# Kernel optimization log

Measured on AMD Instinct MI355X. Metric: run time of the kernel, lower is better.

## Reference

```python
import jax, jax.numpy as jnp
import numpy as np
import math

EMBED_DIM = 128
NUM_HEADS = 16
HEAD_DIM = EMBED_DIM // NUM_HEADS  # = 8 = n_wires of the quantum circuit


def setup_inputs() -> dict:
    key = jax.random.key(0)
    k1, k2, k3 = jax.random.split(key, 3)
    B, S = 4, 2048
    x = jax.random.normal(k1, (B, S, EMBED_DIM), dtype=jnp.float32)
    # shared trainable RX angles of the single q_layer (applied to every head)
    theta = jax.random.normal(k2, (HEAD_DIM,), dtype=jnp.float32)
    w_out = jax.random.normal(k3, (EMBED_DIM, EMBED_DIM), dtype=jnp.float32) / math.sqrt(EMBED_DIM)
    mask = jnp.ones((B, S), dtype=jnp.int32)
    return {"x": x, "theta": theta, "w_out": w_out, "mask": mask}


def quantum_linear(x_head, theta):
    # Circuit: RX(x_i) encode + RX(theta_i) on wire i, CNOT chain (i, i+1),
    # then <Z_j>. For product state |psi_i> = RX(phi_i)|0>, <Z_i> = cos(phi_i),
    # and the CNOT chain gives final <Z_j> = prod_{i<=j} cos(phi_i).
    phi = x_head + theta  # [..., D] broadcast over leading dims
    return jnp.cumprod(jnp.cos(phi), axis=-1)


def reference(x, theta, w_out, mask):
    B, S, E = x.shape
    H, D = NUM_HEADS, HEAD_DIM
    xs = x.reshape(B, S, H, D)
    q = quantum_linear(xs, theta).transpose(0, 2, 1, 3)  # [B, H, S, D]; k = v = q
    scores = jnp.einsum("bhsd,bhtd->bhst", q, q) / math.sqrt(D)
    scores = jnp.where(mask[:, None, None, :] == 0, -1e9, scores)
    probs = jax.nn.softmax(scores, axis=-1)  # dropout is identity in eval
    attn = jnp.einsum("bhst,bhtd->bhsd", probs, q)
    attn = attn.transpose(0, 2, 1, 3).reshape(B, S, E)
    return attn @ w_out.T
```

## Files before the change

kernel.cpp:

```cpp
#include <hip/hip_runtime.h>
#include <hip/hip_bf16.h>
#include <hip/hip_fp16.h>

#define NB 4
#define NS 2048
#define NE 128
#define NH 16
#define ND 8

#define THALF 1024
#define NCH 32
#define VSTRIDE 1032
#define VGSTR 2056

typedef __attribute__((ext_vector_type(8))) _Float16 half8;
typedef __attribute__((ext_vector_type(4))) _Float16 half4;
typedef __attribute__((ext_vector_type(4))) float f32x4;

__device__ __forceinline__ unsigned int pkrtz(float a, float b) {
    typedef __fp16 fp16v2 __attribute__((ext_vector_type(2)));
    union { fp16v2 h; unsigned int u; } v;
    v.h = __builtin_amdgcn_cvt_pkrtz(a, b);
    return v.u;
}
__device__ __forceinline__ unsigned short f2h(float a) {
    return __half_as_ushort(__float2half(a));
}
__device__ __forceinline__ half8 mk_half8(unsigned u0, unsigned u1,
                                          unsigned u2, unsigned u3) {
    union { half8 h; unsigned u[4]; } v;
    v.u[0] = u0; v.u[1] = u1; v.u[2] = u2; v.u[3] = u3;
    return v.h;
}

__device__ __forceinline__ void qrow(const float* __restrict__ xp,
                                     const float* th, float* p) {
    float4 a = *(const float4*)xp, c = *(const float4*)(xp + 4);
    float t = 1.f;
    t *= cosf(a.x + th[0]); p[0] = t;
    t *= cosf(a.y + th[1]); p[1] = t;
    t *= cosf(a.z + th[2]); p[2] = t;
    t *= cosf(a.w + th[3]); p[3] = t;
    t *= cosf(c.x + th[4]); p[4] = t;
    t *= cosf(c.y + th[5]); p[5] = t;
    t *= cosf(c.z + th[6]); p[6] = t;
    t *= cosf(c.w + th[7]); p[7] = t;
}

__global__ __launch_bounds__(256) void qgen_kernel(
        const float* __restrict__ x,
        const float* __restrict__ theta,
        const int* __restrict__ mask,
        const float* __restrict__ w,
        unsigned short* __restrict__ qg,
        unsigned short* __restrict__ vtg,
        unsigned short* __restrict__ wf16) {
    const int gid = blockIdx.x * 256 + threadIdx.x;
    const int bh = gid >> 10;
    const int b = bh >> 4, h = bh & (NH - 1);
    const int j = gid & 1023;
    const int s0 = 2 * j;
    const float SC = 0.71421629f;

    if (blockIdx.x == 0) {
        for (int i = threadIdx.x; i < 2048; i += 256) {
            const float* wp = w + i * 8;
            float4 a = *(const float4*)wp, c = *(const float4*)(wp + 4);
            uint4 pk;
            pk.x = pkrtz(a.x, a.y); pk.y = pkrtz(a.z, a.w);
            pk.z = pkrtz(c.x, c.y); pk.w = pkrtz(c.z, c.w);
            *(uint4*)&wf16[i * 8] = pk;
        }
    }

    float th[ND];
#pragma unroll
    for (int d = 0; d < ND; d++) th[d] = theta[d];

    float p0[ND], p1[ND];
    qrow(x + ((size_t)(b * NS + s0) * NE + h * ND), th, p0);
    qrow(x + ((size_t)(b * NS + s0 + 1) * NE + h * ND), th, p1);
    const float mz0 = mask[b * NS + s0] ? 1.f : 0.f;
    const float mz1 = mask[b * NS + s0 + 1] ? 1.f : 0.f;

    uint4 qa, qb;
    qa.x = pkrtz(p0[0] * SC, p0[1] * SC);
    qa.y = pkrtz(p0[2] * SC, p0[3] * SC);
    qa.z = pkrtz(p0[4] * SC, p0[5] * SC);
    qa.w = pkrtz(p0[6] * SC, p0[7] * SC);
    qb.x = pkrtz(p1[0] * SC, p1[1] * SC);
    qb.y = pkrtz(p1[2] * SC, p1[3] * SC);
    qb.z = pkrtz(p1[4] * SC, p1[5] * SC);
    qb.w = pkrtz(p1[6] * SC, p1[7] * SC);
    *(uint4*)&qg[((size_t)bh * NS + s0) * ND] = qa;
    *(uint4*)&qg[((size_t)bh * NS + s0 + 1) * ND] = qb;

    const int H = s0 >> 10, r0 = s0 & 1023;
    const int chs = r0 >> 5, u = (r0 & 31) >> 1;
    const int i = (u & 1) | (((u >> 3) & 1) << 1) | (((u >> 1) & 3) << 2);
    const int col = H * THALF + chs * 32 + 2 * i;
    unsigned short* vb = vtg + (size_t)bh * 9 * VGSTR + col;
#pragma unroll
    for (int d = 0; d < ND; d++)
        *(unsigned int*)&vb[d * VGSTR] = pkrtz(p0[d] * mz0, p1[d] * mz1);
    *(unsigned int*)&vb[8 * VGSTR] = pkrtz(mz0, mz1);
}

__global__ __launch_bounds__(512) void attn_kernel(
        const unsigned short* __restrict__ qg,
        const unsigned short* __restrict__ vtg,
        unsigned short* __restrict__ mid) {
    __shared__ unsigned short qhl[THALF * ND + 24];
    __shared__ unsigned short vT[9 * VSTRIDE];

    const int bid = blockIdx.x;
    const int bh = bid >> 4;
    const int b = bh >> 4, h = bh & (NH - 1);
    const int msix = bid & 15;
    const int tid = threadIdx.x;

    const int wave = tid >> 6, lane = tid & 63;
    const int quad = lane >> 4, l15 = lane & 15;
    const int mbase = msix * 128 + wave * 16;

    if (tid < 24) qhl[THALF * ND + tid] = 0;

    half4 hz4 = {0, 0, 0, 0};
    const unsigned short* qmrow = qg + ((size_t)bh * NS + mbase + l15) * ND
                                + (quad < 2 ? quad * 4 : 0);
    half4 bm0 = (quad < 2) ? *(const half4*)qmrow : hz4;

    const int vrow = (l15 < 9) ? l15 : 8;
    const unsigned short* vbase = &vT[vrow * VSTRIDE];

    f32x4 O0 = {0.f, 0.f, 0.f, 0.f};
    const f32x4 zc = {0.f, 0.f, 0.f, 0.f};

    for (int p = 0; p < 2; p++) {
        {
            const uint4* qs = (const uint4*)(qg + ((size_t)bh * NS + p * THALF) * ND);
            uint4* qd = (uint4*)qhl;
            qd[tid] = qs[tid];
            qd[tid + 512] = qs[tid + 512];
        }
        {
            const unsigned short* vs = vtg + (size_t)bh * 9 * VGSTR + p * THALF;
            for (int jj = tid; jj < 1152; jj += 512) {
                int d = jj >> 7, c = (jj & 127) << 3;
                *(uint4*)&vT[d * VSTRIDE + c] = *(const uint4*)&vs[d * VGSTR + c];
            }
        }
        __syncthreads();

        for (int ch = 0; ch < NCH; ch++) {
            int tb = ch * 32;
            half4 at0 = *(const half4*)&qhl[(tb + l15) * ND + quad * 4];
            half4 at1 = *(const half4*)&qhl[(tb + 16 + l15) * ND + quad * 4];
            half8 vf  = *(const half8*)&vbase[tb + quad * 8];

            f32x4 s00 = __builtin_amdgcn_mfma_f32_16x16x16f16(at0, bm0, zc, 0, 0, 0);
            f32x4 s10 = __builtin_amdgcn_mfma_f32_16x16x16f16(at1, bm0, zc, 0, 0, 0);

            half8 pA0 = mk_half8(
                pkrtz(__builtin_amdgcn_exp2f(s00[0]), __builtin_amdgcn_exp2f(s00[1])),
                pkrtz(__builtin_amdgcn_exp2f(s00[2]), __builtin_amdgcn_exp2f(s00[3])),
                pkrtz(__builtin_amdgcn_exp2f(s10[0]), __builtin_amdgcn_exp2f(s10[1])),
                pkrtz(__builtin_amdgcn_exp2f(s10[2]), __builtin_amdgcn_exp2f(s10[3])));

            O0 = __builtin_amdgcn_mfma_f32_16x16x32_f16(pA0, vf, O0, 0, 0, 0);
        }
        __syncthreads();
    }

#pragma unroll
    for (int r = 0; r < 4; r++) {
        float lsum = __shfl(O0[r], (lane & 48) | 8, 64);
        float v = O0[r] / lsum;
        if (l15 < ND) {
            int m = mbase + quad * 4 + r;
            mid[(size_t)(b * NS + m) * NE + h * ND + l15] = f2h(v);
        }
    }
}

__global__ __launch_bounds__(512) void proj_kernel(
        const unsigned short* __restrict__ mid,
        const unsigned short* __restrict__ wf16,
        float* __restrict__ out) {
    const int rb = blockIdx.x * 16;
    const int tid = threadIdx.x;
    const int wavei = tid >> 6, lane = tid & 63;
    const int quad = lane >> 4, l15 = lane & 15;
    const int n0 = wavei * 16;

    f32x4 acc = {0.f, 0.f, 0.f, 0.f};
#pragma unroll
    for (int kt = 0; kt < 4; kt++) {
        half8 af = *(const half8*)&mid[(size_t)(rb + l15) * NE + kt * 32 + quad * 8];
        half8 bf = *(const half8*)&wf16[(n0 + l15) * NE + kt * 32 + quad * 8];
        acc = __builtin_amdgcn_mfma_f32_16x16x32_f16(af, bf, acc, 0, 0, 0);
    }
#pragma unroll
    for (int r = 0; r < 4; r++)
        out[(size_t)(rb + quad * 4 + r) * NE + n0 + l15] = acc[r];
}

extern "C" void kernel_launch(void* const* d_in, const int* in_sizes, int n_in,
                              void* d_out, int out_size, void* d_ws, size_t ws_size,
                              hipStream_t stream) {
    const float* x     = (const float*)d_in[0];
    const float* theta = (const float*)d_in[1];
    const float* w_out = (const float*)d_in[2];
    const int*   mask  = (const int*)d_in[3];
    float* out = (float*)d_out;

    unsigned short* mid16 = (unsigned short*)d_ws;
    unsigned short* qg   = mid16 + (size_t)NB * NS * NE;
    unsigned short* vtg  = qg + (size_t)NB * NH * NS * ND;
    unsigned short* wf16 = vtg + (size_t)NB * NH * 9 * VGSTR;

    qgen_kernel<<<NB * NH * NS / 2 / 256, 256, 0, stream>>>(x, theta, mask, w_out,
                                                            qg, vtg, wf16);
    attn_kernel<<<NB * NH * 16, 512, 0, stream>>>(qg, vtg, mid16);
    proj_kernel<<<NB * NS / 16, 512, 0, stream>>>(mid16, wf16, out);
}
```

Before: 103.9 us.

## Switch attention to 32x32x16 MFMA tiles reading K/V directly from global

The attention kernel now uses 32x32x16 f16 MFMA instructions: each wave handles 32 query rows and processes 32 keys per step over 64 steps. LDS staging and the __syncthreads barriers are dropped, and the 256-thread block loads Q and V fragments straight from global memory, relying on L1/L2 caching. The V-transpose layout written by qgen is reorganized into 16-key blocks of 144 halfs so each lane's fragment is contiguous. Global loads in the inner loop may add latency compared with LDS reads, but the larger tiles do more work per instruction and the block no longer has to synchronize.

```diff
diff --git a/kernel.cpp b/kernel.cpp
--- a/kernel.cpp
+++ b/kernel.cpp
@@ -8,14 +8,12 @@
 #define NH 16
 #define ND 8
 
-#define THALF 1024
-#define NCH 32
-#define VSTRIDE 1032
-#define VGSTR 2056
+#define VT_BLK 144
+#define VT_BH (128 * VT_BLK)
 
 typedef __attribute__((ext_vector_type(8))) _Float16 half8;
-typedef __attribute__((ext_vector_type(4))) _Float16 half4;
 typedef __attribute__((ext_vector_type(4))) float f32x4;
+typedef __attribute__((ext_vector_type(16))) float f32x16;
 
 __device__ __forceinline__ unsigned int pkrtz(float a, float b) {
     typedef __fp16 fp16v2 __attribute__((ext_vector_type(2)));
@@ -95,24 +93,19 @@
     *(uint4*)&qg[((size_t)bh * NS + s0) * ND] = qa;
     *(uint4*)&qg[((size_t)bh * NS + s0 + 1) * ND] = qb;
 
-    const int H = s0 >> 10, r0 = s0 & 1023;
-    const int chs = r0 >> 5, u = (r0 & 31) >> 1;
-    const int i = (u & 1) | (((u >> 3) & 1) << 1) | (((u >> 1) & 3) << 2);
-    const int col = H * THALF + chs * 32 + 2 * i;
-    unsigned short* vb = vtg + (size_t)bh * 9 * VGSTR + col;
+    const int blk = s0 >> 4, u = s0 & 15;
+    const int k2 = (u & 3) | (((u >> 3) & 1) << 2) | (((u >> 2) & 1) << 3);
+    unsigned short* vb = vtg + (size_t)bh * VT_BH + blk * VT_BLK + k2;
 #pragma unroll
     for (int d = 0; d < ND; d++)
-        *(unsigned int*)&vb[d * VGSTR] = pkrtz(p0[d] * mz0, p1[d] * mz1);
-    *(unsigned int*)&vb[8 * VGSTR] = pkrtz(mz0, mz1);
-}
-
-__global__ __launch_bounds__(512) void attn_kernel(
+        *(unsigned int*)&vb[d * 16] = pkrtz(p0[d] * mz0, p1[d] * mz1);
+    *(unsigned int*)&vb[8 * 16] = pkrtz(mz0, mz1);
+}
+
+__global__ __launch_bounds__(256) void attn_kernel(
         const unsigned short* __restrict__ qg,
         const unsigned short* __restrict__ vtg,
         unsigned short* __restrict__ mid) {
-    __shared__ unsigned short qhl[THALF * ND + 24];
-    __shared__ unsigned short vT[9 * VSTRIDE];
-
     const int bid = blockIdx.x;
     const int bh = bid >> 4;
     const int b = bh >> 4, h = bh & (NH - 1);
@@ -120,65 +113,48 @@
     const int tid = threadIdx.x;
 
     const int wave = tid >> 6, lane = tid & 63;
-    const int quad = lane >> 4, l15 = lane & 15;
-    const int mbase = msix * 128 + wave * 16;
-
-    if (tid < 24) qhl[THALF * ND + tid] = 0;
-
-    half4 hz4 = {0, 0, 0, 0};
-    const unsigned short* qmrow = qg + ((size_t)bh * NS + mbase + l15) * ND
-                                + (quad < 2 ? quad * 4 : 0);
-    half4 bm0 = (quad < 2) ? *(const half4*)qmrow : hz4;
-
-    const int vrow = (l15 < 9) ? l15 : 8;
-    const unsigned short* vbase = &vT[vrow * VSTRIDE];
-
-    f32x4 O0 = {0.f, 0.f, 0.f, 0.f};
-    const f32x4 zc = {0.f, 0.f, 0.f, 0.f};
-
-    for (int p = 0; p < 2; p++) {
-        {
-            const uint4* qs = (const uint4*)(qg + ((size_t)bh * NS + p * THALF) * ND);
-            uint4* qd = (uint4*)qhl;
-            qd[tid] = qs[tid];
-            qd[tid + 512] = qs[tid + 512];
-        }
-        {
-            const unsigned short* vs = vtg + (size_t)bh * 9 * VGSTR + p * THALF;
-            for (int jj = tid; jj < 1152; jj += 512) {
-                int d = jj >> 7, c = (jj & 127) << 3;
-                *(uint4*)&vT[d * VSTRIDE + c] = *(const uint4*)&vs[d * VGSTR + c];
-            }
-        }
-        __syncthreads();
-
-        for (int ch = 0; ch < NCH; ch++) {
-            int tb = ch * 32;
-            half4 at0 = *(const half4*)&qhl[(tb + l15) * ND + quad * 4];
-            half4 at1 = *(const half4*)&qhl[(tb + 16 + l15) * ND + quad * 4];
-            half8 vf  = *(const half8*)&vbase[tb + quad * 8];
-
-            f32x4 s00 = __builtin_amdgcn_mfma_f32_16x16x16f16(at0, bm0, zc, 0, 0, 0);
-            f32x4 s10 = __builtin_amdgcn_mfma_f32_16x16x16f16(at1, bm0, zc, 0, 0, 0);
-
-            half8 pA0 = mk_half8(
-                pkrtz(__builtin_amdgcn_exp2f(s00[0]), __builtin_amdgcn_exp2f(s00[1])),
-                pkrtz(__builtin_amdgcn_exp2f(s00[2]), __builtin_amdgcn_exp2f(s00[3])),
-                pkrtz(__builtin_amdgcn_exp2f(s10[0]), __builtin_amdgcn_exp2f(s10[1])),
-                pkrtz(__builtin_amdgcn_exp2f(s10[2]), __builtin_amdgcn_exp2f(s10[3])));
-
-            O0 = __builtin_amdgcn_mfma_f32_16x16x32_f16(pA0, vf, O0, 0, 0, 0);
-        }
-        __syncthreads();
-    }
-
-#pragma unroll
-    for (int r = 0; r < 4; r++) {
-        float lsum = __shfl(O0[r], (lane & 48) | 8, 64);
-        float v = O0[r] / lsum;
-        if (l15 < ND) {
-            int m = mbase + quad * 4 + r;
-            mid[(size_t)(b * NS + m) * NE + h * ND + l15] = f2h(v);
+    const int l31 = lane & 31, hi = lane >> 5;
+    const int mb = msix * 128 + wave * 32;
+
+    half8 hz = {0, 0, 0, 0, 0, 0, 0, 0};
+    half8 bm = hi ? hz : *(const half8*)&qg[((size_t)bh * NS + mb + l31) * ND];
+
+    const unsigned short* qt = qg + (size_t)bh * NS * ND + (size_t)l31 * ND;
+    const int dv = (l31 < 9) ? l31 : 8;
+    const unsigned short* vb = vtg + (size_t)bh * VT_BH + dv * 16 + hi * 8;
+
+    f32x16 O = {0.f};
+    const f32x16 zc = {0.f};
+
+    for (int ch = 0; ch < 64; ch++) {
+        half8 at = *(const half8*)&qt[(size_t)ch * 32 * ND];
+        half8 vf1 = *(const half8*)&vb[ch * 2 * VT_BLK];
+        half8 vf2 = *(const half8*)&vb[ch * 2 * VT_BLK + VT_BLK];
+
+        f32x16 s = __builtin_amdgcn_mfma_f32_32x32x16_f16(at, bm, zc, 0, 0, 0);
+
+        half8 pA1 = mk_half8(
+            pkrtz(__builtin_amdgcn_exp2f(s[0]),  __builtin_amdgcn_exp2f(s[1])),
+            pkrtz(__builtin_amdgcn_exp2f(s[2]),  __builtin_amdgcn_exp2f(s[3])),
+            pkrtz(__builtin_amdgcn_exp2f(s[4]),  __builtin_amdgcn_exp2f(s[5])),
+            pkrtz(__builtin_amdgcn_exp2f(s[6]),  __builtin_amdgcn_exp2f(s[7])));
+        half8 pA2 = mk_half8(
+            pkrtz(__builtin_amdgcn_exp2f(s[8]),  __builtin_amdgcn_exp2f(s[9])),
+            pkrtz(__builtin_amdgcn_exp2f(s[10]), __builtin_amdgcn_exp2f(s[11])),
+            pkrtz(__builtin_amdgcn_exp2f(s[12]), __builtin_amdgcn_exp2f(s[13])),
+            pkrtz(__builtin_amdgcn_exp2f(s[14]), __builtin_amdgcn_exp2f(s[15])));
+
+        O = __builtin_amdgcn_mfma_f32_32x32x16_f16(pA1, vf1, O, 0, 0, 0);
+        O = __builtin_amdgcn_mfma_f32_32x32x16_f16(pA2, vf2, O, 0, 0, 0);
+    }
+
+#pragma unroll
+    for (int r = 0; r < 16; r++) {
+        float lsum = __shfl(O[r], (lane & 32) | 8, 64);
+        float v = O[r] / lsum;
+        if (l31 < ND) {
+            int m = mb + (r & 3) + 8 * (r >> 2) + 4 * hi;
+            mid[(size_t)(b * NS + m) * NE + h * ND + l31] = f2h(v);
         }
     }
 }
@@ -217,10 +193,10 @@
     unsigned short* mid16 = (unsigned short*)d_ws;
     unsigned short* qg   = mid16 + (size_t)NB * NS * NE;
     unsigned short* vtg  = qg + (size_t)NB * NH * NS * ND;
-    unsigned short* wf16 = vtg + (size_t)NB * NH * 9 * VGSTR;
+    unsigned short* wf16 = vtg + (size_t)NB * NH * VT_BH;
 
     qgen_kernel<<<NB * NH * NS / 2 / 256, 256, 0, stream>>>(x, theta, mask, w_out,
                                                             qg, vtg, wf16);
-    attn_kernel<<<NB * NH * 16, 512, 0, stream>>>(qg, vtg, mid16);
+    attn_kernel<<<NB * NH * 16, 256, 0, stream>>>(qg, vtg, mid16);
     proj_kernel<<<NB * NS / 16, 512, 0, stream>>>(mid16, wf16, out);
 }
```

Result: slower. 110.1 us (+5.9%).
